# Optimization experiments

Hardware: AMD Instinct MI355X
Metric: run time of the kernel (lower is better)

Reference implementation:

```python
import jax, jax.numpy as jnp
import numpy as np

B = 131072
DIM = 64
D_IN = 32
D_OUT = 32
HIDDEN = 512
N_BINS = 8
TAIL = 3.0


def setup_inputs() -> dict:
    key = jax.random.key(0)
    ks = jax.random.split(key, 7)
    x = jax.random.normal(ks[0], (B, DIM), dtype=jnp.float32)
    out_dim = D_OUT * (3 * N_BINS - 1)  # 32 * 23 = 736
    W1 = jax.random.normal(ks[1], (D_IN, HIDDEN), dtype=jnp.float32) / np.sqrt(D_IN)
    b1 = jnp.zeros((HIDDEN,), dtype=jnp.float32)
    W2 = jax.random.normal(ks[2], (HIDDEN, HIDDEN), dtype=jnp.float32) / np.sqrt(HIDDEN)
    b2 = jnp.zeros((HIDDEN,), dtype=jnp.float32)
    W3 = jax.random.normal(ks[3], (HIDDEN, out_dim), dtype=jnp.float32) / np.sqrt(HIDDEN)
    b3 = jnp.zeros((out_dim,), dtype=jnp.float32)
    return {"x": x, "W1": W1, "b1": b1, "W2": W2, "b2": b2, "W3": W3, "b3": b3}


def _gather(t, idx):
    # t: (..., K), idx: (...) -> (...,)
    return jnp.take_along_axis(t, idx[..., None], axis=-1)[..., 0]


def rq_spline_forward(x, widths, heights, derivatives, tail_bound=TAIL):
    K = widths.shape[-1]
    widths = jax.nn.softmax(widths, axis=-1) * 2 * tail_bound
    heights = jax.nn.softmax(heights, axis=-1) * 2 * tail_bound
    derivatives = jax.nn.softplus(derivatives)
    ones = jnp.ones_like(derivatives[..., :1])
    derivatives = jnp.concatenate([ones, derivatives, ones], axis=-1)  # (..., K+1)
    cumwidths = jnp.cumsum(widths, axis=-1)
    cumwidths = jnp.pad(cumwidths, [(0, 0)] * (cumwidths.ndim - 1) + [(1, 0)]) - tail_bound
    cumheights = jnp.cumsum(heights, axis=-1)
    cumheights = jnp.pad(cumheights, [(0, 0)] * (cumheights.ndim - 1) + [(1, 0)]) - tail_bound

    inside = (x >= -tail_bound) & (x <= tail_bound)
    xc = jnp.clip(x, -tail_bound + 1e-6, tail_bound - 1e-6)
    # searchsorted (left): number of knots strictly less than xc
    bin_idx = jnp.sum(cumwidths[..., 1:] < xc[..., None], axis=-1)
    bin_idx = jnp.clip(bin_idx, 0, K - 1)

    w_k = _gather(widths, bin_idx)
    h_k = _gather(heights, bin_idx)
    d_k = _gather(derivatives, bin_idx)
    d_k1 = _gather(derivatives[..., 1:], bin_idx)
    cw_k = _gather(cumwidths, bin_idx)
    ch_k = _gather(cumheights, bin_idx)

    xi = jnp.clip((xc - cw_k) / w_k, 1e-6, 1 - 1e-6)
    s_k = h_k / w_k
    num = h_k * (s_k * xi**2 + d_k * xi * (1 - xi))
    den = s_k + (d_k + d_k1 - 2 * s_k) * xi * (1 - xi)
    y_inside = ch_k + num / den
    log_det_inside = (
        jnp.log(s_k**2 * (d_k1 * xi**2 + 2 * s_k * xi * (1 - xi) + d_k * (1 - xi) ** 2) + 1e-8)
        - jnp.log(den**2 + 1e-8)
    )
    y = jnp.where(inside, y_inside, x)
    log_det = jnp.where(inside, log_det_inside, jnp.zeros_like(x))
    return y, log_det


def reference(x, W1, b1, W2, b2, W3, b3):
    # mask: first D_IN dims conditioned on, last D_OUT transformed
    x_masked = x[:, :D_IN]
    x_transform = x[:, D_IN:]
    h = jax.nn.relu(x_masked @ W1 + b1)
    h = jax.nn.relu(h @ W2 + b2)
    raw = h @ W3 + b3
    raw = raw.reshape(x.shape[0], D_OUT, 3 * N_BINS - 1)
    widths = raw[..., :N_BINS]
    heights = raw[..., N_BINS:2 * N_BINS]
    derivs = raw[..., 2 * N_BINS:]
    y_t, log_det = rq_spline_forward(x_transform, widths, heights, derivs, TAIL)
    y = jnp.concatenate([x_masked, y_t], axis=-1)
    return y, jnp.sum(log_det, axis=-1)
```

## Files before the change

kernel.cpp:

```cpp
#include <hip/hip_runtime.h>
#include <hip/hip_bf16.h>
#include <stdint.h>

typedef __bf16 bf16_t;
typedef _Float16 f16_t;
typedef _Float16 f16x8 __attribute__((ext_vector_type(8)));
typedef _Float16 f16x4 __attribute__((ext_vector_type(4)));
typedef float f32x4 __attribute__((ext_vector_type(4)));

#define HID 512
#define NRAW 736
#define NRAW_PAD 768
#define TAILB 3.0f

__device__ __forceinline__ void glds16(const void* g, void* s) {
  __builtin_amdgcn_global_load_lds(
      (const __attribute__((address_space(1))) void*)g,
      (__attribute__((address_space(3))) void*)s, 16, 0, 0);
}
__device__ __forceinline__ float frcp(float x) { return __builtin_amdgcn_rcpf(x); }

__global__ void detect_dtype(const void* x, int* flag) {
  __shared__ int s;
  if (threadIdx.x == 0) s = 0;
  __syncthreads();
  const bf16_t* xb = (const bf16_t*)x;
  int cnt = 0;
  for (int j = 0; j < 16; j++) {
    float v = (float)xb[threadIdx.x * 16 + j];
    if (!(v == v) || fabsf(v) > 64.0f) cnt++;
  }
  atomicAdd(&s, cnt);
  __syncthreads();
  if (threadIdx.x == 0) *flag = (s > 64) ? 1 : 0;
}

__global__ void conv_wb(const void* W1, const void* W2, const void* W3,
                        const void* b1, const void* b2, const void* b3,
                        f16_t* __restrict__ w1t, f16_t* __restrict__ w2t,
                        f16_t* __restrict__ w3t,
                        float* __restrict__ bf1, float* __restrict__ bf2,
                        float* __restrict__ bf3, const int* flagp) {
  const int flag = *flagp;
  auto rd = [&](const void* p, size_t idx) -> float {
    return flag ? ((const float*)p)[idx] : (float)((const bf16_t*)p)[idx];
  };
  int i = blockIdx.x * 256 + threadIdx.x;
  if (i < 512 * 32)  { w1t[i] = (f16_t)rd(W1, (size_t)(i & 31) * 512 + (i >> 5)); return; }
  i -= 512 * 32;
  if (i < 512 * 512) { w2t[i] = (f16_t)rd(W2, (size_t)(i & 511) * 512 + (i >> 9)); return; }
  i -= 512 * 512;
  if (i < NRAW_PAD * 512) {
    int n = i >> 9, k = i & 511;
    int ch = n / 24, e = n % 24;
    w3t[i] = (e < 23) ? (f16_t)rd(W3, (size_t)k * NRAW + ch * 23 + e) : (f16_t)0.0f;
    return;
  }
  i -= NRAW_PAD * 512;
  if (i < 512) { bf1[i] = rd(b1, i); return; }
  i -= 512;
  if (i < 512) { bf2[i] = rd(b2, i); return; }
  i -= 512;
  if (i < NRAW_PAD) {
    int ch = i / 24, e = i % 24;
    bf3[i] = (e < 23) ? rd(b3, (size_t)ch * 23 + e) : 0.0f;
  }
}

__global__ void convert_x(const void* x, void* __restrict__ outv,
                          const int* flagp, int n) {
  const int flag = *flagp;
  const int i0 = (blockIdx.x * 256 + threadIdx.x) * 8;
  if (i0 >= n) return;
  const int row = i0 >> 5, col = i0 & 31;
  const size_t src = (size_t)row * 64 + col;
  if (flag) {
    const float4* s4 = (const float4*)((const float*)x + src);
    float4* d4 = (float4*)((float*)outv + src);
    d4[0] = s4[0]; d4[1] = s4[1];
  } else {
    *(uint4*)((bf16_t*)outv + src) = *(const uint4*)((const bf16_t*)x + src);
  }
}

__global__ void ld_finalize(const float* __restrict__ ldp, void* __restrict__ outv,
                            const int* __restrict__ flagp, int M) {
  const int i = blockIdx.x * 256 + threadIdx.x;
  if (i >= M) return;
  float s = 0.f;
  #pragma unroll
  for (int n = 0; n < 4; n++) s += ldp[(size_t)n * M + i];
  if (*flagp) ((float*)outv)[(size_t)M * 64 + i] = s;
  else        ((bf16_t*)outv)[(size_t)M * 64 + i] = (bf16_t)s;
}

__launch_bounds__(512, 4)
__global__ void gemm12(const void* __restrict__ xorig, const f16_t* __restrict__ W1t,
                       const float* __restrict__ b1, const f16_t* __restrict__ W2t,
                       const float* __restrict__ b2, f16_t* __restrict__ H2,
                       int r0, const int* __restrict__ flagp) {
  constexpr int BK = 64;
  constexpr int BUF = 128 * BK;
  __shared__ __align__(16) f16_t As[2 * BUF], Bs[2 * BUF];
  const int t = threadIdx.x;
  const int id = blockIdx.x;
  const int xcd = id & 7, s = id >> 3;
  const int n0 = (s & 3) * 128;
  const int m0 = ((s >> 2) * 8 + xcd) * 128;
  const int lrow = t >> 3, lcb = t & 7;
  const int lane = t & 63, w = t >> 6;
  const int wr = (w >> 2) * 64;
  const int wc = (w & 3) * 32;
  const int wc4 = (w & 3) * 16;
  const int lm = lane & 15, quad = lane >> 4;
  const int flag = *flagp;

  const f16_t* gb[2];
  f16_t* ldb[2];
  #pragma unroll
  for (int r = 0; r < 2; r++) {
    const int row = r * 64 + lrow;
    const int gc = (lcb ^ (row & 7)) * 8;
    gb[r] = W2t + (size_t)(n0 + row) * 512 + gc;
    ldb[r] = &Bs[row * BK + lcb * 8];
  }
  int apo[4][2], bpo[2][2];
  #pragma unroll
  for (int ksi = 0; ksi < 2; ksi++) {
    const int qb = ksi * 4 + quad;
    #pragma unroll
    for (int i = 0; i < 4; i++) {
      const int ra = wr + i * 16 + lm;
      apo[i][ksi] = ra * BK + ((qb ^ (ra & 7)) << 3);
    }
    #pragma unroll
    for (int j = 0; j < 2; j++) {
      const int rb = wc + j * 16 + lm;
      bpo[j][ksi] = rb * BK + ((qb ^ (rb & 7)) << 3);
    }
  }
  f16x8 xfr[4];
  #pragma unroll
  for (int i = 0; i < 4; i++) {
    const size_t xrow = (size_t)(r0 + m0 + wr + i * 16 + lm);
    if (flag) {
      const float* px = (const float*)xorig + xrow * 64 + quad * 8;
      const float4 a = *(const float4*)px;
      const float4 b = *(const float4*)(px + 4);
      f16x8 v;
      v[0] = (f16_t)a.x; v[1] = (f16_t)a.y; v[2] = (f16_t)a.z; v[3] = (f16_t)a.w;
      v[4] = (f16_t)b.x; v[5] = (f16_t)b.y; v[6] = (f16_t)b.z; v[7] = (f16_t)b.w;
      xfr[i] = v;
    } else {
      const bf16_t* px = (const bf16_t*)xorig + xrow * 64 + quad * 8;
      f16x8 v;
      #pragma unroll
      for (int j = 0; j < 8; j++) v[j] = (f16_t)(float)px[j];
      xfr[i] = v;
    }
  }
  const f16_t* w1p = W1t + (size_t)(wc4 + lm) * 32 + quad * 8;
  const float* b1p = b1 + wc4 + 4 * quad;
  int woff[4];
  {
    const int cb = (w & 3) * 2 + (quad >> 1);
    #pragma unroll
    for (int i = 0; i < 4; i++) {
      const int row = wr + i * 16 + lm;
      woff[i] = row * BK + ((cb ^ (row & 7)) << 3) + 4 * (quad & 1);
    }
  }

  f32x4 acc[4][2] = {};

  #pragma unroll
  for (int r = 0; r < 2; r++) glds16(gb[r], ldb[r]);
  {
    const f16x8 w1f = *(const f16x8*)w1p;
    const float4 bv = *(const float4*)b1p;
    #pragma unroll
    for (int i = 0; i < 4; i++) {
      f32x4 z = {};
      const f32x4 h = __builtin_amdgcn_mfma_f32_16x16x32_f16(w1f, xfr[i], z, 0, 0, 0);
      f16x4 v;
      v[0] = (f16_t)fmaxf(h[0] + bv.x, 0.0f);
      v[1] = (f16_t)fmaxf(h[1] + bv.y, 0.0f);
      v[2] = (f16_t)fmaxf(h[2] + bv.z, 0.0f);
      v[3] = (f16_t)fmaxf(h[3] + bv.w, 0.0f);
      *(f16x4*)&As[woff[i]] = v;
    }
  }
  f16x8 w1fa = *(const f16x8*)(w1p + (size_t)64 * 32);
  float4 bva = *(const float4*)(b1p + 64);
  __syncthreads();

  #pragma unroll
  for (int k = 0; k < 8; k++) {
    const int cur = k & 1, nb = cur ^ 1;
    if (k < 7) {
      #pragma unroll
      for (int r = 0; r < 2; r++)
        glds16(gb[r] + (k + 1) * 64, ldb[r] + nb * BUF);
    }
    f32x4 h[4];
    if (k < 7) {
      #pragma unroll
      for (int i = 0; i < 4; i++) {
        f32x4 z = {};
        h[i] = __builtin_amdgcn_mfma_f32_16x16x32_f16(w1fa, xfr[i], z, 0, 0, 0);
      }
    }
    #pragma unroll
    for (int ksi = 0; ksi < 2; ksi++) {
      f16x8 af[4], bf[2];
      #pragma unroll
      for (int i = 0; i < 4; i++) af[i] = *(const f16x8*)&As[cur * BUF + apo[i][ksi]];
      #pragma unroll
      for (int j = 0; j < 2; j++) bf[j] = *(const f16x8*)&Bs[cur * BUF + bpo[j][ksi]];
      __builtin_amdgcn_s_setprio(1);
      #pragma unroll
      for (int i = 0; i < 4; i++)
        #pragma unroll
        for (int j = 0; j < 2; j++)
          acc[i][j] = __builtin_amdgcn_mfma_f32_16x16x32_f16(af[i], bf[j], acc[i][j], 0, 0, 0);
      __builtin_amdgcn_s_setprio(0);
    }
    if (k < 7) {
      #pragma unroll
      for (int i = 0; i < 4; i++) {
        f16x4 v;
        v[0] = (f16_t)fmaxf(h[i][0] + bva.x, 0.0f);
        v[1] = (f16_t)fmaxf(h[i][1] + bva.y, 0.0f);
        v[2] = (f16_t)fmaxf(h[i][2] + bva.z, 0.0f);
        v[3] = (f16_t)fmaxf(h[i][3] + bva.w, 0.0f);
        *(f16x4*)&As[nb * BUF + woff[i]] = v;
      }
      if (k < 6) {
        w1fa = *(const f16x8*)(w1p + (size_t)(k + 2) * 64 * 32);
        bva = *(const float4*)(b1p + (k + 2) * 64);
      }
      __syncthreads();
    }
  }
  #pragma unroll
  for (int i = 0; i < 4; i++)
    #pragma unroll
    for (int j = 0; j < 2; j++) {
      const int col = n0 + wc + j * 16 + lm;
      const float bv = b2[col];
      #pragma unroll
      for (int r = 0; r < 4; r++) {
        const int rowi = m0 + wr + i * 16 + quad * 4 + r;
        H2[(size_t)rowi * HID + col] = (f16_t)fmaxf(acc[i][j][r] + bv, 0.0f);
      }
    }
}

#define RSH 200
#define SP1 0.5413248546f

__launch_bounds__(512, 4)
__global__ void gemm3_spline(const f16_t* __restrict__ A, const f16_t* __restrict__ Bt,
                             const float* __restrict__ bias,
                             const void* __restrict__ xorig,
                             void* __restrict__ outv, float* __restrict__ ldp,
                             int M, int r0, const int* __restrict__ flagp) {
  __shared__ __align__(16) f16_t lds[2 * 8192 + 2 * 12288];
  f16_t* As = lds;
  f16_t* Bs = lds + 2 * 8192;
  f16_t* rawh = lds;

  const int t = threadIdx.x;
  const int id = blockIdx.x;
  const int xcd = id & 7, sloc = id >> 3;
  const int cpx = gridDim.x >> 3;
  const int wg = xcd * cpx + sloc;
  const int ntile = wg & 3;
  const int m0 = (wg >> 2) * 128;
  const int n0 = ntile * 192;
  const int lane = t & 63, w = t >> 6;
  const int lm = lane & 15, quad = lane >> 4;
  const int wrow = (w >> 2) * 64, wcol = (w & 3) * 48;
  const int lrow = t >> 3, lcb = t & 7;
  const int flag = *flagp;

  const int gc = (lcb ^ (lrow & 7)) * 8;
  const f16_t* gA = A + (size_t)(m0 + lrow) * 512 + gc;
  const f16_t* gB = Bt + (size_t)(n0 + lrow) * 512 + gc;
  f16_t* ldA = As + lrow * 64 + lcb * 8;
  f16_t* ldB = Bs + lrow * 64 + lcb * 8;

  int aoff[4], boff[3];
  #pragma unroll
  for (int i = 0; i < 4; i++) {
    const int ra = wrow + i * 16 + lm;
    aoff[i] = ra * 64 + ((quad ^ (ra & 7)) << 3);
  }
  #pragma unroll
  for (int j = 0; j < 3; j++) {
    const int rb = wcol + j * 16 + lm;
    boff[j] = rb * 64 + ((quad ^ (rb & 7)) << 3);
  }

  const int prow = t >> 3, pch = t & 7;
  float xt_pre[2];
  #pragma unroll
  for (int e = 0; e < 2; e++) {
    const size_t gi = (size_t)(r0 + m0 + e * 64 + prow) * 64 + 32 + ntile * 8 + pch;
    xt_pre[e] = flag ? ((const float*)xorig)[gi] : (float)((const bf16_t*)xorig)[gi];
  }
  float bv3[3];
  #pragma unroll
  for (int j = 0; j < 3; j++) bv3[j] = bias[n0 + wcol + j * 16 + lm];

  #pragma unroll
  for (int r = 0; r < 2; r++) glds16(gA + r * 32768, ldA + r * 4096);
  #pragma unroll
  for (int r = 0; r < 3; r++) glds16(gB + r * 32768, ldB + r * 4096);
  __syncthreads();

  f32x4 acc[4][3] = {};

  #pragma unroll
  for (int t8 = 0; t8 < 8; t8++) {
    const f16_t* Ab = As + (t8 & 1) * 8192;
    const f16_t* Bb = Bs + (t8 & 1) * 12288;
    if (t8 < 7) {
      const int nb = (t8 + 1) & 1;
      #pragma unroll
      for (int r = 0; r < 2; r++)
        glds16(gA + r * 32768 + (t8 + 1) * 64, ldA + nb * 8192 + r * 4096);
      #pragma unroll
      for (int r = 0; r < 3; r++)
        glds16(gB + r * 32768 + (t8 + 1) * 64, ldB + nb * 12288 + r * 4096);
    }
    #pragma unroll
    for (int ksi = 0; ksi < 2; ksi++) {
      f16x8 af[4], bf[3];
      #pragma unroll
      for (int i = 0; i < 4; i++)
        af[i] = *(const f16x8*)(Ab + (aoff[i] ^ (ksi << 5)));
      #pragma unroll
      for (int j = 0; j < 3; j++)
        bf[j] = *(const f16x8*)(Bb + (boff[j] ^ (ksi << 5)));
      __builtin_amdgcn_s_setprio(1);
      #pragma unroll
      for (int i = 0; i < 4; i++)
        #pragma unroll
        for (int j = 0; j < 3; j++)
          acc[i][j] = __builtin_amdgcn_mfma_f32_16x16x32_f16(af[i], bf[j], acc[i][j], 0, 0, 0);
      __builtin_amdgcn_s_setprio(0);
    }
    __syncthreads();
  }

  #pragma unroll
  for (int i = 0; i < 4; i++)
    #pragma unroll
    for (int j = 0; j < 3; j++) {
      const int col = wcol + j * 16 + lm;
      #pragma unroll
      for (int r = 0; r < 4; r++)
        rawh[(wrow + i * 16 + quad * 4 + r) * RSH + col] = (f16_t)(acc[i][j][r] + bv3[j]);
    }
  __syncthreads();

  #pragma unroll
  for (int e = 0; e < 2; e++) {
    const int row = e * 64 + prow;
    const f16_t* c16 = &rawh[row * RSH + pch * 24];
    const f16x8 v0 = *(const f16x8*)(c16);
    const f16x8 v1 = *(const f16x8*)(c16 + 8);
    const f16x8 v2 = *(const f16x8*)(c16 + 16);
    float wa[8], ha[8], da[7];
    #pragma unroll
    for (int j = 0; j < 8; j++) { wa[j] = (float)v0[j]; ha[j] = (float)v1[j]; }
    #pragma unroll
    for (int j = 0; j < 7; j++) da[j] = (float)v2[j];

    const float xt = xt_pre[e];
    const bool inside = (xt >= -TAILB) && (xt <= TAILB);
    const float xc = fminf(fmaxf(xt, -TAILB + 1e-6f), TAILB - 1e-6f);

    float mw = wa[0], mh = ha[0];
    #pragma unroll
    for (int j = 1; j < 8; j++) { mw = fmaxf(mw, wa[j]); mh = fmaxf(mh, ha[j]); }
    float ew[8], eh[8], sew = 0.f, seh = 0.f;
    #pragma unroll
    for (int j = 0; j < 8; j++) {
      ew[j] = __expf(wa[j] - mw); sew += ew[j];
      eh[j] = __expf(ha[j] - mh); seh += eh[j];
    }
    const float wsc = 6.0f * frcp(sew), hsc = 6.0f * frcp(seh);
    #pragma unroll
    for (int j = 0; j < 8; j++) { ew[j] *= wsc; eh[j] *= hsc; }

    float accw = -TAILB, runh = -TAILB;
    float cwk = -TAILB, chk = -TAILB;
    float wk = ew[0], hk = eh[0];
    float dkr = SP1, dk1r = da[0];
    #pragma unroll
    for (int i = 0; i < 7; i++) {
      accw += ew[i];
      runh += eh[i];
      const bool cond = accw < xc;
      cwk  = cond ? accw : cwk;
      chk  = cond ? runh : chk;
      wk   = cond ? ew[i + 1] : wk;
      hk   = cond ? eh[i + 1] : hk;
      dkr  = cond ? da[i] : dkr;
      dk1r = cond ? ((i == 6) ? SP1 : da[i + 1]) : dk1r;
    }
    const float dk  = fmaxf(dkr, 0.0f)  + __logf(1.0f + __expf(-fabsf(dkr)));
    const float dk1 = fmaxf(dk1r, 0.0f) + __logf(1.0f + __expf(-fabsf(dk1r)));

    const float rwk = frcp(wk);
    float xi = (xc - cwk) * rwk;
    xi = fminf(fmaxf(xi, 1e-6f), 1.0f - 1e-6f);
    const float om = 1.0f - xi;
    const float sl = hk * rwk;
    const float num = hk * (sl * xi * xi + dk * xi * om);
    const float den = sl + (dk + dk1 - 2.0f * sl) * xi * om;
    const float y_in = chk + num * frcp(den);
    const float t1 = sl * sl * (dk1 * xi * xi + 2.0f * sl * xi * om + dk * om * om);
    const float ld_in = __logf(t1 + 1e-8f) - __logf(den * den + 1e-8f);

    const float yv = inside ? y_in : xt;
    const float ldv = inside ? ld_in : 0.0f;

    const size_t grow = (size_t)(r0 + m0 + row);
    if (flag) ((float*)outv)[grow * 64 + 32 + ntile * 8 + pch] = yv;
    else      ((bf16_t*)outv)[grow * 64 + 32 + ntile * 8 + pch] = (bf16_t)yv;

    float l = ldv + __shfl_down(ldv, 1, 8);
    l += __shfl_down(l, 2, 8);
    l += __shfl_down(l, 4, 8);
    if ((t & 7) == 0) ldp[(size_t)ntile * M + grow] = l;
  }
}

extern "C" void kernel_launch(void* const* d_in, const int* in_sizes, int n_in,
                              void* d_out, int out_size, void* d_ws, size_t ws_size,
                              hipStream_t stream) {
  const void* x  = d_in[0];
  const void* W1 = d_in[1];
  const void* b1 = d_in[2];
  const void* W2 = d_in[3];
  const void* b2 = d_in[4];
  const void* W3 = d_in[5];
  const void* b3 = d_in[6];
  const int M = in_sizes[0] / 64;

  char* ws = (char*)d_ws;
  size_t off = 0;
  auto alloc = [&](size_t bytes) {
    void* p = ws + off;
    off += (bytes + 255) & ~(size_t)255;
    return p;
  };
  int*   flag = (int*)alloc(256);
  float* bf1  = (float*)alloc(512 * 4);
  float* bf2  = (float*)alloc(512 * 4);
  float* bf3  = (float*)alloc(NRAW_PAD * 4);
  f16_t* W1t  = (f16_t*)alloc((size_t)512 * 32 * 2);
  f16_t* W2t  = (f16_t*)alloc((size_t)512 * 512 * 2);
  f16_t* W3t  = (f16_t*)alloc((size_t)NRAW_PAD * 512 * 2);
  float* ldp  = (float*)alloc((size_t)8 * M * 4);

  const size_t per_row = (size_t)HID * 2;
  size_t avail = (ws_size > off + 4096) ? (ws_size - off - 4096) : 0;
  long rows = (long)(avail / per_row);
  rows -= rows % 1024;
  if (rows > M) rows = M;
  if (rows < 1024) rows = 1024;

  f16_t* h2 = (f16_t*)alloc((size_t)rows * HID * 2);

  detect_dtype<<<1, 256, 0, stream>>>(x, flag);
  conv_wb<<<2631, 256, 0, stream>>>(W1, W2, W3, b1, b2, b3,
                                    W1t, W2t, W3t, bf1, bf2, bf3, flag);
  convert_x<<<(M * 32 / 8 + 255) / 256, 256, 0, stream>>>(x, d_out, flag, M * 32);

  for (int r0 = 0; r0 < M; r0 += (int)rows) {
    const int mc = (int)((M - r0 < rows) ? (M - r0) : rows);
    const int mt128 = mc / 128;
    gemm12<<<mt128 * 4, 512, 0, stream>>>(x, W1t, bf1, W2t, bf2, h2, r0, flag);
    gemm3_spline<<<mt128 * 4, 512, 0, stream>>>(
        h2, W3t, bf3, x, d_out, ldp, M, r0, flag);
  }
  ld_finalize<<<(M + 255) / 256, 256, 0, stream>>>(ldp, d_out, flag, M);
}
```

Baseline: 320.5 us.

## Triple-buffer the gemm3_spline LDS pipeline with prefetch distance two

Moves the third GEMM's K-loop from double to triple buffering in LDS, issuing global-to-LDS loads two tiles ahead. Each iteration now waits on the vector-memory counter explicitly and uses one raw s_barrier instead of a trailing __syncthreads, so load latency has more time to hide behind MFMA work. The cost is a larger LDS footprint (about 120 KB instead of 80 KB) and launch bounds lowered from 4 to 2, which cuts how many blocks can be resident per CU.

```diff
diff --git a/kernel.cpp b/kernel.cpp
--- a/kernel.cpp
+++ b/kernel.cpp
@@ -258,16 +258,15 @@
 
 #define RSH 200
 #define SP1 0.5413248546f
-
-__launch_bounds__(512, 4)
+#define G3BUF 20480
+
+__launch_bounds__(512, 2)
 __global__ void gemm3_spline(const f16_t* __restrict__ A, const f16_t* __restrict__ Bt,
                              const float* __restrict__ bias,
                              const void* __restrict__ xorig,
                              void* __restrict__ outv, float* __restrict__ ldp,
                              int M, int r0, const int* __restrict__ flagp) {
-  __shared__ __align__(16) f16_t lds[2 * 8192 + 2 * 12288];
-  f16_t* As = lds;
-  f16_t* Bs = lds + 2 * 8192;
+  __shared__ __align__(16) f16_t lds[3 * G3BUF];
   f16_t* rawh = lds;
 
   const int t = threadIdx.x;
@@ -287,8 +286,7 @@
   const int gc = (lcb ^ (lrow & 7)) * 8;
   const f16_t* gA = A + (size_t)(m0 + lrow) * 512 + gc;
   const f16_t* gB = Bt + (size_t)(n0 + lrow) * 512 + gc;
-  f16_t* ldA = As + lrow * 64 + lcb * 8;
-  f16_t* ldB = Bs + lrow * 64 + lcb * 8;
+  const int lslot = lrow * 64 + lcb * 8;
 
   int aoff[4], boff[3];
   #pragma unroll
@@ -299,7 +297,7 @@
   #pragma unroll
   for (int j = 0; j < 3; j++) {
     const int rb = wcol + j * 16 + lm;
-    boff[j] = rb * 64 + ((quad ^ (rb & 7)) << 3);
+    boff[j] = 8192 + rb * 64 + ((quad ^ (rb & 7)) << 3);
   }
 
   const int prow = t >> 3, pch = t & 7;
@@ -313,33 +311,43 @@
   #pragma unroll
   for (int j = 0; j < 3; j++) bv3[j] = bias[n0 + wcol + j * 16 + lm];
 
-  #pragma unroll
-  for (int r = 0; r < 2; r++) glds16(gA + r * 32768, ldA + r * 4096);
-  #pragma unroll
-  for (int r = 0; r < 3; r++) glds16(gB + r * 32768, ldB + r * 4096);
-  __syncthreads();
+  asm volatile("s_waitcnt vmcnt(0)" ::: "memory");
+  __builtin_amdgcn_sched_barrier(0);
+
+  #pragma unroll
+  for (int r = 0; r < 2; r++) glds16(gA + r * 32768,       lds + lslot + r * 4096);
+  #pragma unroll
+  for (int r = 0; r < 3; r++) glds16(gB + r * 32768,       lds + 8192 + lslot + r * 4096);
+  #pragma unroll
+  for (int r = 0; r < 2; r++) glds16(gA + r * 32768 + 64,  lds + G3BUF + lslot + r * 4096);
+  #pragma unroll
+  for (int r = 0; r < 3; r++) glds16(gB + r * 32768 + 64,  lds + G3BUF + 8192 + lslot + r * 4096);
 
   f32x4 acc[4][3] = {};
 
   #pragma unroll
   for (int t8 = 0; t8 < 8; t8++) {
-    const f16_t* Ab = As + (t8 & 1) * 8192;
-    const f16_t* Bb = Bs + (t8 & 1) * 12288;
-    if (t8 < 7) {
-      const int nb = (t8 + 1) & 1;
+    if (t8 == 7) asm volatile("s_waitcnt vmcnt(0)" ::: "memory");
+    else         asm volatile("s_waitcnt vmcnt(5)" ::: "memory");
+    __builtin_amdgcn_sched_barrier(0);
+    __builtin_amdgcn_s_barrier();
+    __builtin_amdgcn_sched_barrier(0);
+    if (t8 < 6) {
+      const int nb = (t8 + 2) % 3;
       #pragma unroll
       for (int r = 0; r < 2; r++)
-        glds16(gA + r * 32768 + (t8 + 1) * 64, ldA + nb * 8192 + r * 4096);
+        glds16(gA + r * 32768 + (t8 + 2) * 64, lds + nb * G3BUF + lslot + r * 4096);
       #pragma unroll
       for (int r = 0; r < 3; r++)
-        glds16(gB + r * 32768 + (t8 + 1) * 64, ldB + nb * 12288 + r * 4096);
-    }
+        glds16(gB + r * 32768 + (t8 + 2) * 64, lds + nb * G3BUF + 8192 + lslot + r * 4096);
+    }
+    const f16_t* Bb = lds + (t8 % 3) * G3BUF;
     #pragma unroll
     for (int ksi = 0; ksi < 2; ksi++) {
       f16x8 af[4], bf[3];
       #pragma unroll
       for (int i = 0; i < 4; i++)
-        af[i] = *(const f16x8*)(Ab + (aoff[i] ^ (ksi << 5)));
+        af[i] = *(const f16x8*)(Bb + (aoff[i] ^ (ksi << 5)));
       #pragma unroll
       for (int j = 0; j < 3; j++)
         bf[j] = *(const f16x8*)(Bb + (boff[j] ^ (ksi << 5)));
@@ -351,8 +359,9 @@
           acc[i][j] = __builtin_amdgcn_mfma_f32_16x16x32_f16(af[i], bf[j], acc[i][j], 0, 0, 0);
       __builtin_amdgcn_s_setprio(0);
     }
-    __syncthreads();
-  }
+  }
+
+  __syncthreads();
 
   #pragma unroll
   for (int i = 0; i < 4; i++)
```

Result: slower. 364.8 us (+13.8%).

## Merge GEMM12 and GEMM3+spline into one software-pipelined kernel over row chunks

Applied to the files above, without the earlier changes.

Both GEMM stages are fused into a single kernel where even blocks run layers 1-2 for chunk c and odd blocks run layer 3 plus the spline for chunk c-1. A double-buffered H2 workspace lets the two stages overlap within one launch instead of running as back-to-back dependent launches. The aim is to fill the device with mixed work and hide each stage's tail. The costs are a fixed 16384-row chunk, extra launches for pipeline fill and drain, and a larger shared-memory footprint for the GEMM12 role.

```diff
diff --git a/kernel.cpp b/kernel.cpp
--- a/kernel.cpp
+++ b/kernel.cpp
@@ -94,348 +94,348 @@
   else        ((bf16_t*)outv)[(size_t)M * 64 + i] = (bf16_t)s;
 }
 
+#define RSH 200
+#define SP1 0.5413248546f
+
 __launch_bounds__(512, 4)
-__global__ void gemm12(const void* __restrict__ xorig, const f16_t* __restrict__ W1t,
-                       const float* __restrict__ b1, const f16_t* __restrict__ W2t,
-                       const float* __restrict__ b2, f16_t* __restrict__ H2,
-                       int r0, const int* __restrict__ flagp) {
-  constexpr int BK = 64;
-  constexpr int BUF = 128 * BK;
-  __shared__ __align__(16) f16_t As[2 * BUF], Bs[2 * BUF];
+__global__ void gemm_pipe(const void* __restrict__ xorig,
+                          const f16_t* __restrict__ W1t, const float* __restrict__ b1,
+                          const f16_t* __restrict__ W2t, const float* __restrict__ b2,
+                          f16_t* __restrict__ h2w, const f16_t* __restrict__ h2r,
+                          const f16_t* __restrict__ W3t, const float* __restrict__ bf3v,
+                          void* __restrict__ outv, float* __restrict__ ldp,
+                          int M, int g12r0, int g3r0, int nb12, int nb3,
+                          const int* __restrict__ flagp) {
+  __shared__ __align__(16) f16_t lds[40960];
   const int t = threadIdx.x;
-  const int id = blockIdx.x;
-  const int xcd = id & 7, s = id >> 3;
-  const int n0 = (s & 3) * 128;
-  const int m0 = ((s >> 2) * 8 + xcd) * 128;
+  const int role = blockIdx.x & 1;
+  const int sid = blockIdx.x >> 1;
+  const int lane = t & 63, w = t >> 6;
+  const int lm = lane & 15, quad = lane >> 4;
   const int lrow = t >> 3, lcb = t & 7;
-  const int lane = t & 63, w = t >> 6;
-  const int wr = (w >> 2) * 64;
-  const int wc = (w & 3) * 32;
-  const int wc4 = (w & 3) * 16;
-  const int lm = lane & 15, quad = lane >> 4;
   const int flag = *flagp;
 
-  const f16_t* gb[2];
-  f16_t* ldb[2];
-  #pragma unroll
-  for (int r = 0; r < 2; r++) {
-    const int row = r * 64 + lrow;
-    const int gc = (lcb ^ (row & 7)) * 8;
-    gb[r] = W2t + (size_t)(n0 + row) * 512 + gc;
-    ldb[r] = &Bs[row * BK + lcb * 8];
-  }
-  int apo[4][2], bpo[2][2];
-  #pragma unroll
-  for (int ksi = 0; ksi < 2; ksi++) {
-    const int qb = ksi * 4 + quad;
+  if (role == 0) {
+    if (g12r0 < 0 || sid >= nb12) return;
+    constexpr int BK = 64;
+    constexpr int BUF = 128 * BK;
+    f16_t* As = lds;
+    f16_t* Bs = lds + 2 * BUF;
+    const int xcd = sid & 7, s = sid >> 3;
+    const int n0 = (s & 3) * 128;
+    const int m0 = ((s >> 2) * 8 + xcd) * 128;
+    const int wr = (w >> 2) * 64;
+    const int wc = (w & 3) * 32;
+    const int wc4 = (w & 3) * 16;
+    const int r0 = g12r0;
+
+    const f16_t* gb[2];
+    f16_t* ldb[2];
+    #pragma unroll
+    for (int r = 0; r < 2; r++) {
+      const int row = r * 64 + lrow;
+      const int gc = (lcb ^ (row & 7)) * 8;
+      gb[r] = W2t + (size_t)(n0 + row) * 512 + gc;
+      ldb[r] = &Bs[row * BK + lcb * 8];
+    }
+    int apo[4][2], bpo[2][2];
+    #pragma unroll
+    for (int ksi = 0; ksi < 2; ksi++) {
+      const int qb = ksi * 4 + quad;
+      #pragma unroll
+      for (int i = 0; i < 4; i++) {
+        const int ra = wr + i * 16 + lm;
+        apo[i][ksi] = ra * BK + ((qb ^ (ra & 7)) << 3);
+      }
+      #pragma unroll
+      for (int j = 0; j < 2; j++) {
+        const int rb = wc + j * 16 + lm;
+        bpo[j][ksi] = rb * BK + ((qb ^ (rb & 7)) << 3);
+      }
+    }
+    f16x8 xfr[4];
     #pragma unroll
     for (int i = 0; i < 4; i++) {
-      const int ra = wr + i * 16 + lm;
-      apo[i][ksi] = ra * BK + ((qb ^ (ra & 7)) << 3);
-    }
-    #pragma unroll
-    for (int j = 0; j < 2; j++) {
-      const int rb = wc + j * 16 + lm;
-      bpo[j][ksi] = rb * BK + ((qb ^ (rb & 7)) << 3);
-    }
-  }
-  f16x8 xfr[4];
-  #pragma unroll
-  for (int i = 0; i < 4; i++) {
-    const size_t xrow = (size_t)(r0 + m0 + wr + i * 16 + lm);
-    if (flag) {
-      const float* px = (const float*)xorig + xrow * 64 + quad * 8;
-      const float4 a = *(const float4*)px;
-      const float4 b = *(const float4*)(px + 4);
-      f16x8 v;
-      v[0] = (f16_t)a.x; v[1] = (f16_t)a.y; v[2] = (f16_t)a.z; v[3] = (f16_t)a.w;
-      v[4] = (f16_t)b.x; v[5] = (f16_t)b.y; v[6] = (f16_t)b.z; v[7] = (f16_t)b.w;
-      xfr[i] = v;
-    } else {
-      const bf16_t* px = (const bf16_t*)xorig + xrow * 64 + quad * 8;
-      f16x8 v;
-      #pragma unroll
-      for (int j = 0; j < 8; j++) v[j] = (f16_t)(float)px[j];
-      xfr[i] = v;
-    }
-  }
-  const f16_t* w1p = W1t + (size_t)(wc4 + lm) * 32 + quad * 8;
-  const float* b1p = b1 + wc4 + 4 * quad;
-  int woff[4];
-  {
-    const int cb = (w & 3) * 2 + (quad >> 1);
-    #pragma unroll
-    for (int i = 0; i < 4; i++) {
-      const int row = wr + i * 16 + lm;
-      woff[i] = row * BK + ((cb ^ (row & 7)) << 3) + 4 * (quad & 1);
-    }
-  }
-
-  f32x4 acc[4][2] = {};
-
-  #pragma unroll
-  for (int r = 0; r < 2; r++) glds16(gb[r], ldb[r]);
-  {
-    const f16x8 w1f = *(const f16x8*)w1p;
-    const float4 bv = *(const float4*)b1p;
-    #pragma unroll
-    for (int i = 0; i < 4; i++) {
-      f32x4 z = {};
-      const f32x4 h = __builtin_amdgcn_mfma_f32_16x16x32_f16(w1f, xfr[i], z, 0, 0, 0);
-      f16x4 v;
-      v[0] = (f16_t)fmaxf(h[0] + bv.x, 0.0f);
-      v[1] = (f16_t)fmaxf(h[1] + bv.y, 0.0f);
-      v[2] = (f16_t)fmaxf(h[2] + bv.z, 0.0f);
-      v[3] = (f16_t)fmaxf(h[3] + bv.w, 0.0f);
-      *(f16x4*)&As[woff[i]] = v;
-    }
-  }
-  f16x8 w1fa = *(const f16x8*)(w1p + (size_t)64 * 32);
-  float4 bva = *(const float4*)(b1p + 64);
-  __syncthreads();
-
-  #pragma unroll
-  for (int k = 0; k < 8; k++) {
-    const int cur = k & 1, nb = cur ^ 1;
-    if (k < 7) {
-      #pragma unroll
-      for (int r = 0; r < 2; r++)
-        glds16(gb[r] + (k + 1) * 64, ldb[r] + nb * BUF);
-    }
-    f32x4 h[4];
-    if (k < 7) {
+      const size_t xrow = (size_t)(r0 + m0 + wr + i * 16 + lm);
+      if (flag) {
+        const float* px = (const float*)xorig + xrow * 64 + quad * 8;
+        const float4 a = *(const float4*)px;
+        const float4 b = *(const float4*)(px + 4);
+        f16x8 v;
+        v[0] = (f16_t)a.x; v[1] = (f16_t)a.y; v[2] = (f16_t)a.z; v[3] = (f16_t)a.w;
+        v[4] = (f16_t)b.x; v[5] = (f16_t)b.y; v[6] = (f16_t)b.z; v[7] = (f16_t)b.w;
+        xfr[i] = v;
+      } else {
+        const bf16_t* px = (const bf16_t*)xorig + xrow * 64 + quad * 8;
+        f16x8 v;
+        #pragma unroll
+        for (int j = 0; j < 8; j++) v[j] = (f16_t)(float)px[j];
+        xfr[i] = v;
+      }
+    }
+    const f16_t* w1p = W1t + (size_t)(wc4 + lm) * 32 + quad * 8;
+    const float* b1p = b1 + wc4 + 4 * quad;
+    int woff[4];
+    {
+      const int cb = (w & 3) * 2 + (quad >> 1);
+      #pragma unroll
+      for (int i = 0; i < 4; i++) {
+        const int row = wr + i * 16 + lm;
+        woff[i] = row * BK + ((cb ^ (row & 7)) << 3) + 4 * (quad & 1);
+      }
+    }
+
+    f32x4 acc[4][2] = {};
+
+    #pragma unroll
+    for (int r = 0; r < 2; r++) glds16(gb[r], ldb[r]);
+    {
+      const f16x8 w1f = *(const f16x8*)w1p;
+      const float4 bv = *(const float4*)b1p;
       #pragma unroll
       for (int i = 0; i < 4; i++) {
         f32x4 z = {};
-        h[i] = __builtin_amdgcn_mfma_f32_16x16x32_f16(w1fa, xfr[i], z, 0, 0, 0);
-      }
-    }
-    #pragma unroll
-    for (int ksi = 0; ksi < 2; ksi++) {
-      f16x8 af[4], bf[2];
-      #pragma unroll
-      for (int i = 0; i < 4; i++) af[i] = *(const f16x8*)&As[cur * BUF + apo[i][ksi]];
-      #pragma unroll
-      for (int j = 0; j < 2; j++) bf[j] = *(const f16x8*)&Bs[cur * BUF + bpo[j][ksi]];
-      __builtin_amdgcn_s_setprio(1);
-      #pragma unroll
-      for (int i = 0; i < 4; i++)
-        #pragma unroll
-        for (int j = 0; j < 2; j++)
-          acc[i][j] = __builtin_amdgcn_mfma_f32_16x16x32_f16(af[i], bf[j], acc[i][j], 0, 0, 0);
-      __builtin_amdgcn_s_setprio(0);
-    }
-    if (k < 7) {
-      #pragma unroll
-      for (int i = 0; i < 4; i++) {
+        const f32x4 h = __builtin_amdgcn_mfma_f32_16x16x32_f16(w1f, xfr[i], z, 0, 0, 0);
         f16x4 v;
-        v[0] = (f16_t)fmaxf(h[i][0] + bva.x, 0.0f);
-        v[1] = (f16_t)fmaxf(h[i][1] + bva.y, 0.0f);
-        v[2] = (f16_t)fmaxf(h[i][2] + bva.z, 0.0f);
-        v[3] = (f16_t)fmaxf(h[i][3] + bva.w, 0.0f);
-        *(f16x4*)&As[nb * BUF + woff[i]] = v;
-      }
-      if (k < 6) {
-        w1fa = *(const f16x8*)(w1p + (size_t)(k + 2) * 64 * 32);
-        bva = *(const float4*)(b1p + (k + 2) * 64);
+        v[0] = (f16_t)fmaxf(h[0] + bv.x, 0.0f);
+        v[1] = (f16_t)fmaxf(h[1] + bv.y, 0.0f);
+        v[2] = (f16_t)fmaxf(h[2] + bv.z, 0.0f);
+        v[3] = (f16_t)fmaxf(h[3] + bv.w, 0.0f);
+        *(f16x4*)&As[woff[i]] = v;
+      }
+    }
+    f16x8 w1fa = *(const f16x8*)(w1p + (size_t)64 * 32);
+    float4 bva = *(const float4*)(b1p + 64);
+    __syncthreads();
+
+    #pragma unroll
+    for (int k = 0; k < 8; k++) {
+      const int cur = k & 1, nb = cur ^ 1;
+      if (k < 7) {
+        #pragma unroll
+        for (int r = 0; r < 2; r++)
+          glds16(gb[r] + (k + 1) * 64, ldb[r] + nb * BUF);
+      }
+      f32x4 h[4];
+      if (k < 7) {
+        #pragma unroll
+        for (int i = 0; i < 4; i++) {
+          f32x4 z = {};
+          h[i] = __builtin_amdgcn_mfma_f32_16x16x32_f16(w1fa, xfr[i], z, 0, 0, 0);
+        }
+      }
+      #pragma unroll
+      for (int ksi = 0; ksi < 2; ksi++) {
+        f16x8 af[4], bf[2];
+        #pragma unroll
+        for (int i = 0; i < 4; i++) af[i] = *(const f16x8*)&As[cur * BUF + apo[i][ksi]];
+        #pragma unroll
+        for (int j = 0; j < 2; j++) bf[j] = *(const f16x8*)&Bs[cur * BUF + bpo[j][ksi]];
+        __builtin_amdgcn_s_setprio(1);
+        #pragma unroll
+        for (int i = 0; i < 4; i++)
+          #pragma unroll
+          for (int j = 0; j < 2; j++)
+            acc[i][j] = __builtin_amdgcn_mfma_f32_16x16x32_f16(af[i], bf[j], acc[i][j], 0, 0, 0);
+        __builtin_amdgcn_s_setprio(0);
+      }
+      if (k < 7) {
+        #pragma unroll
+        for (int i = 0; i < 4; i++) {
+          f16x4 v;
+          v[0] = (f16_t)fmaxf(h[i][0] + bva.x, 0.0f);
+          v[1] = (f16_t)fmaxf(h[i][1] + bva.y, 0.0f);
+          v[2] = (f16_t)fmaxf(h[i][2] + bva.z, 0.0f);
+          v[3] = (f16_t)fmaxf(h[i][3] + bva.w, 0.0f);
+          *(f16x4*)&As[nb * BUF + woff[i]] = v;
+        }
+        if (k < 6) {
+          w1fa = *(const f16x8*)(w1p + (size_t)(k + 2) * 64 * 32);
+          bva = *(const float4*)(b1p + (k + 2) * 64);
+        }
+        __syncthreads();
+      }
+    }
+    #pragma unroll
+    for (int i = 0; i < 4; i++)
+      #pragma unroll
+      for (int j = 0; j < 2; j++) {
+        const int col = n0 + wc + j * 16 + lm;
+        const float bv = b2[col];
+        #pragma unroll
+        for (int r = 0; r < 4; r++) {
+          const int rowi = m0 + wr + i * 16 + quad * 4 + r;
+          h2w[(size_t)rowi * HID + col] = (f16_t)fmaxf(acc[i][j][r] + bv, 0.0f);
+        }
+      }
+  } else {
+    if (g3r0 < 0 || sid >= nb3) return;
+    f16_t* As = lds;
+    f16_t* Bs = lds + 2 * 8192;
+    f16_t* rawh = lds;
+    const int nsub = gridDim.x >> 1;
+    const int xcd = sid & 7, sloc = sid >> 3;
+    const int cpx = nsub >> 3;
+    const int wg = xcd * cpx + sloc;
+    const int ntile = wg & 3;
+    const int m0 = (wg >> 2) * 128;
+    const int n0 = ntile * 192;
+    const int wrow = (w >> 2) * 64, wcol = (w & 3) * 48;
+    const int r0 = g3r0;
+
+    const int gc = (lcb ^ (lrow & 7)) * 8;
+    const f16_t* gA = h2r + (size_t)(m0 + lrow) * 512 + gc;
+    const f16_t* gB = W3t + (size_t)(n0 + lrow) * 512 + gc;
+    f16_t* ldA = As + lrow * 64 + lcb * 8;
+    f16_t* ldB = Bs + lrow * 64 + lcb * 8;
+
+    int aoff[4], boff[3];
+    #pragma unroll
+    for (int i = 0; i < 4; i++) {
+      const int ra = wrow + i * 16 + lm;
+      aoff[i] = ra * 64 + ((quad ^ (ra & 7)) << 3);
+    }
+    #pragma unroll
+    for (int j = 0; j < 3; j++) {
+      const int rb = wcol + j * 16 + lm;
+      boff[j] = rb * 64 + ((quad ^ (rb & 7)) << 3);
+    }
+
+    const int prow = t >> 3, pch = t & 7;
+    float xt_pre[2];
+    #pragma unroll
+    for (int e = 0; e < 2; e++) {
+      const size_t gi = (size_t)(r0 + m0 + e * 64 + prow) * 64 + 32 + ntile * 8 + pch;
+      xt_pre[e] = flag ? ((const float*)xorig)[gi] : (float)((const bf16_t*)xorig)[gi];
+    }
+    float bv3[3];
+    #pragma unroll
+    for (int j = 0; j < 3; j++) bv3[j] = bf3v[n0 + wcol + j * 16 + lm];
+
+    #pragma unroll
+    for (int r = 0; r < 2; r++) glds16(gA + r * 32768, ldA + r * 4096);
+    #pragma unroll
+    for (int r = 0; r < 3; r++) glds16(gB + r * 32768, ldB + r * 4096);
+    __syncthreads();
+
+    f32x4 acc[4][3] = {};
+
+    #pragma unroll
+    for (int t8 = 0; t8 < 8; t8++) {
+      const f16_t* Ab = As + (t8 & 1) * 8192;
+      const f16_t* Bb = Bs + (t8 & 1) * 12288;
+      if (t8 < 7) {
+        const int nb = (t8 + 1) & 1;
+        #pragma unroll
+        for (int r = 0; r < 2; r++)
+          glds16(gA + r * 32768 + (t8 + 1) * 64, ldA + nb * 8192 + r * 4096);
+        #pragma unroll
+        for (int r = 0; r < 3; r++)
+          glds16(gB + r * 32768 + (t8 + 1) * 64, ldB + nb * 12288 + r * 4096);
+      }
+      #pragma unroll
+      for (int ksi = 0; ksi < 2; ksi++) {
+        f16x8 af[4], bf[3];
+        #pragma unroll
+        for (int i = 0; i < 4; i++)
+          af[i] = *(const f16x8*)(Ab + (aoff[i] ^ (ksi << 5)));
+        #pragma unroll
+        for (int j = 0; j < 3; j++)
+          bf[j] = *(const f16x8*)(Bb + (boff[j] ^ (ksi << 5)));
+        __builtin_amdgcn_s_setprio(1);
+        #pragma unroll
+        for (int i = 0; i < 4; i++)
+          #pragma unroll
+          for (int j = 0; j < 3; j++)
+            acc[i][j] = __builtin_amdgcn_mfma_f32_16x16x32_f16(af[i], bf[j], acc[i][j], 0, 0, 0);
+        __builtin_amdgcn_s_setprio(0);
       }
       __syncthreads();
     }
-  }
-  #pragma unroll
-  for (int i = 0; i < 4; i++)
-    #pragma unroll
-    for (int j = 0; j < 2; j++) {
-      const int col = n0 + wc + j * 16 + lm;
-      const float bv = b2[col];
-      #pragma unroll
-      for (int r = 0; r < 4; r++) {
-        const int rowi = m0 + wr + i * 16 + quad * 4 + r;
-        H2[(size_t)rowi * HID + col] = (f16_t)fmaxf(acc[i][j][r] + bv, 0.0f);
-      }
-    }
-}
-
-#define RSH 200
-#define SP1 0.5413248546f
-
-__launch_bounds__(512, 4)
-__global__ void gemm3_spline(const f16_t* __restrict__ A, const f16_t* __restrict__ Bt,
-                             const float* __restrict__ bias,
-                             const void* __restrict__ xorig,
-                             void* __restrict__ outv, float* __restrict__ ldp,
-                             int M, int r0, const int* __restrict__ flagp) {
-  __shared__ __align__(16) f16_t lds[2 * 8192 + 2 * 12288];
-  f16_t* As = lds;
-  f16_t* Bs = lds + 2 * 8192;
-  f16_t* rawh = lds;
-
-  const int t = threadIdx.x;
-  const int id = blockIdx.x;
-  const int xcd = id & 7, sloc = id >> 3;
-  const int cpx = gridDim.x >> 3;
-  const int wg = xcd * cpx + sloc;
-  const int ntile = wg & 3;
-  const int m0 = (wg >> 2) * 128;
-  const int n0 = ntile * 192;
-  const int lane = t & 63, w = t >> 6;
-  const int lm = lane & 15, quad = lane >> 4;
-  const int wrow = (w >> 2) * 64, wcol = (w & 3) * 48;
-  const int lrow = t >> 3, lcb = t & 7;
-  const int flag = *flagp;
-
-  const int gc = (lcb ^ (lrow & 7)) * 8;
-  const f16_t* gA = A + (size_t)(m0 + lrow) * 512 + gc;
-  const f16_t* gB = Bt + (size_t)(n0 + lrow) * 512 + gc;
-  f16_t* ldA = As + lrow * 64 + lcb * 8;
-  f16_t* ldB = Bs + lrow * 64 + lcb * 8;
-
-  int aoff[4], boff[3];
-  #pragma unroll
-  for (int i = 0; i < 4; i++) {
-    const int ra = wrow + i * 16 + lm;
-    aoff[i] = ra * 64 + ((quad ^ (ra & 7)) << 3);
-  }
-  #pragma unroll
-  for (int j = 0; j < 3; j++) {
-    const int rb = wcol + j * 16 + lm;
-    boff[j] = rb * 64 + ((quad ^ (rb & 7)) << 3);
-  }
-
-  const int prow = t >> 3, pch = t & 7;
-  float xt_pre[2];
-  #pragma unroll
-  for (int e = 0; e < 2; e++) {
-    const size_t gi = (size_t)(r0 + m0 + e * 64 + prow) * 64 + 32 + ntile * 8 + pch;
-    xt_pre[e] = flag ? ((const float*)xorig)[gi] : (float)((const bf16_t*)xorig)[gi];
-  }
-  float bv3[3];
-  #pragma unroll
-  for (int j = 0; j < 3; j++) bv3[j] = bias[n0 + wcol + j * 16 + lm];
-
-  #pragma unroll
-  for (int r = 0; r < 2; r++) glds16(gA + r * 32768, ldA + r * 4096);
-  #pragma unroll
-  for (int r = 0; r < 3; r++) glds16(gB + r * 32768, ldB + r * 4096);
-  __syncthreads();
-
-  f32x4 acc[4][3] = {};
-
-  #pragma unroll
-  for (int t8 = 0; t8 < 8; t8++) {
-    const f16_t* Ab = As + (t8 & 1) * 8192;
-    const f16_t* Bb = Bs + (t8 & 1) * 12288;
-    if (t8 < 7) {
-      const int nb = (t8 + 1) & 1;
-      #pragma unroll
-      for (int r = 0; r < 2; r++)
-        glds16(gA + r * 32768 + (t8 + 1) * 64, ldA + nb * 8192 + r * 4096);
-      #pragma unroll
-      for (int r = 0; r < 3; r++)
-        glds16(gB + r * 32768 + (t8 + 1) * 64, ldB + nb * 12288 + r * 4096);
-    }
-    #pragma unroll
-    for (int ksi = 0; ksi < 2; ksi++) {
-      f16x8 af[4], bf[3];
-      #pragma unroll
-      for (int i = 0; i < 4; i++)
-        af[i] = *(const f16x8*)(Ab + (aoff[i] ^ (ksi << 5)));
-      #pragma unroll
-      for (int j = 0; j < 3; j++)
-        bf[j] = *(const f16x8*)(Bb + (boff[j] ^ (ksi << 5)));
-      __builtin_amdgcn_s_setprio(1);
-      #pragma unroll
-      for (int i = 0; i < 4; i++)
-        #pragma unroll
-        for (int j = 0; j < 3; j++)
-          acc[i][j] = __builtin_amdgcn_mfma_f32_16x16x32_f16(af[i], bf[j], acc[i][j], 0, 0, 0);
-      __builtin_amdgcn_s_setprio(0);
-    }
+
+    #pragma unroll
+    for (int i = 0; i < 4; i++)
+      #pragma unroll
+      for (int j = 0; j < 3; j++) {
+        const int col = wcol + j * 16 + lm;
+        #pragma unroll
+        for (int r = 0; r < 4; r++)
+          rawh[(wrow + i * 16 + quad * 4 + r) * RSH + col] = (f16_t)(acc[i][j][r] + bv3[j]);
+      }
     __syncthreads();
-  }
-
-  #pragma unroll
-  for (int i = 0; i < 4; i++)
-    #pragma unroll
-    for (int j = 0; j < 3; j++) {
-      const int col = wcol + j * 16 + lm;
-      #pragma unroll
-      for (int r = 0; r < 4; r++)
-        rawh[(wrow + i * 16 + quad * 4 + r) * RSH + col] = (f16_t)(acc[i][j][r] + bv3[j]);
-    }
-  __syncthreads();
-
-  #pragma unroll
-  for (int e = 0; e < 2; e++) {
-    const int row = e * 64 + prow;
-    const f16_t* c16 = &rawh[row * RSH + pch * 24];
-    const f16x8 v0 = *(const f16x8*)(c16);
-    const f16x8 v1 = *(const f16x8*)(c16 + 8);
-    const f16x8 v2 = *(const f16x8*)(c16 + 16);
-    float wa[8], ha[8], da[7];
-    #pragma unroll
-    for (int j = 0; j < 8; j++) { wa[j] = (float)v0[j]; ha[j] = (float)v1[j]; }
-    #pragma unroll
-    for (int j = 0; j < 7; j++) da[j] = (float)v2[j];
-
-    const float xt = xt_pre[e];
-    const bool inside = (xt >= -TAILB) && (xt <= TAILB);
-    const float xc = fminf(fmaxf(xt, -TAILB + 1e-6f), TAILB - 1e-6f);
-
-    float mw = wa[0], mh = ha[0];
-    #pragma unroll
-    for (int j = 1; j < 8; j++) { mw = fmaxf(mw, wa[j]); mh = fmaxf(mh, ha[j]); }
-    float ew[8], eh[8], sew = 0.f, seh = 0.f;
-    #pragma unroll
-    for (int j = 0; j < 8; j++) {
-      ew[j] = __expf(wa[j] - mw); sew += ew[j];
-      eh[j] = __expf(ha[j] - mh); seh += eh[j];
-    }
-    const float wsc = 6.0f * frcp(sew), hsc = 6.0f * frcp(seh);
-    #pragma unroll
-    for (int j = 0; j < 8; j++) { ew[j] *= wsc; eh[j] *= hsc; }
-
-    float accw = -TAILB, runh = -TAILB;
-    float cwk = -TAILB, chk = -TAILB;
-    float wk = ew[0], hk = eh[0];
-    float dkr = SP1, dk1r = da[0];
-    #pragma unroll
-    for (int i = 0; i < 7; i++) {
-      accw += ew[i];
-      runh += eh[i];
-      const bool cond = accw < xc;
-      cwk  = cond ? accw : cwk;
-      chk  = cond ? runh : chk;
-      wk   = cond ? ew[i + 1] : wk;
-      hk   = cond ? eh[i + 1] : hk;
-      dkr  = cond ? da[i] : dkr;
-      dk1r = cond ? ((i == 6) ? SP1 : da[i + 1]) : dk1r;
-    }
-    const float dk  = fmaxf(dkr, 0.0f)  + __logf(1.0f + __expf(-fabsf(dkr)));
-    const float dk1 = fmaxf(dk1r, 0.0f) + __logf(1.0f + __expf(-fabsf(dk1r)));
-
-    const float rwk = frcp(wk);
-    float xi = (xc - cwk) * rwk;
-    xi = fminf(fmaxf(xi, 1e-6f), 1.0f - 1e-6f);
-    const float om = 1.0f - xi;
-    const float sl = hk * rwk;
-    const float num = hk * (sl * xi * xi + dk * xi * om);
-    const float den = sl + (dk + dk1 - 2.0f * sl) * xi * om;
-    const float y_in = chk + num * frcp(den);
-    const float t1 = sl * sl * (dk1 * xi * xi + 2.0f * sl * xi * om + dk * om * om);
-    const float ld_in = __logf(t1 + 1e-8f) - __logf(den * den + 1e-8f);
-
-    const float yv = inside ? y_in : xt;
-    const float ldv = inside ? ld_in : 0.0f;
-
-    const size_t grow = (size_t)(r0 + m0 + row);
-    if (flag) ((float*)outv)[grow * 64 + 32 + ntile * 8 + pch] = yv;
-    else      ((bf16_t*)outv)[grow * 64 + 32 + ntile * 8 + pch] = (bf16_t)yv;
-
-    float l = ldv + __shfl_down(ldv, 1, 8);
-    l += __shfl_down(l, 2, 8);
-    l += __shfl_down(l, 4, 8);
-    if ((t & 7) == 0) ldp[(size_t)ntile * M + grow] = l;
+
+    #pragma unroll
+    for (int e = 0; e < 2; e++) {
+      const int row = e * 64 + prow;
+      const f16_t* c16 = &rawh[row * RSH + pch * 24];
+      const f16x8 v0 = *(const f16x8*)(c16);
+      const f16x8 v1 = *(const f16x8*)(c16 + 8);
+      const f16x8 v2 = *(const f16x8*)(c16 + 16);
+      float wa[8], ha[8], da[7];
+      #pragma unroll
+      for (int j = 0; j < 8; j++) { wa[j] = (float)v0[j]; ha[j] = (float)v1[j]; }
+      #pragma unroll
+      for (int j = 0; j < 7; j++) da[j] = (float)v2[j];
+
+      const float xt = xt_pre[e];
+      const bool inside = (xt >= -TAILB) && (xt <= TAILB);
+      const float xc = fminf(fmaxf(xt, -TAILB + 1e-6f), TAILB - 1e-6f);
+
+      float mw = wa[0], mh = ha[0];
+      #pragma unroll
+      for (int j = 1; j < 8; j++) { mw = fmaxf(mw, wa[j]); mh = fmaxf(mh, ha[j]); }
+      float ew[8], eh[8], sew = 0.f, seh = 0.f;
+      #pragma unroll
+      for (int j = 0; j < 8; j++) {
+        ew[j] = __expf(wa[j] - mw); sew += ew[j];
+        eh[j] = __expf(ha[j] - mh); seh += eh[j];
+      }
+      const float wsc = 6.0f * frcp(sew), hsc = 6.0f * frcp(seh);
+      #pragma unroll
+      for (int j = 0; j < 8; j++) { ew[j] *= wsc; eh[j] *= hsc; }
+
+      float accw = -TAILB, runh = -TAILB;
+      float cwk = -TAILB, chk = -TAILB;
+      float wk = ew[0], hk = eh[0];
+      float dkr = SP1, dk1r = da[0];
+      #pragma unroll
+      for (int i = 0; i < 7; i++) {
+        accw += ew[i];
+        runh += eh[i];
+        const bool cond = accw < xc;
+        cwk  = cond ? accw : cwk;
+        chk  = cond ? runh : chk;
+        wk   = cond ? ew[i + 1] : wk;
+        hk   = cond ? eh[i + 1] : hk;
+        dkr  = cond ? da[i] : dkr;
+        dk1r = cond ? ((i == 6) ? SP1 : da[i + 1]) : dk1r;
+      }
+      const float dk  = fmaxf(dkr, 0.0f)  + __logf(1.0f + __expf(-fabsf(dkr)));
+      const float dk1 = fmaxf(dk1r, 0.0f) + __logf(1.0f + __expf(-fabsf(dk1r)));
+
+      const float rwk = frcp(wk);
+      float xi = (xc - cwk) * rwk;
+      xi = fminf(fmaxf(xi, 1e-6f), 1.0f - 1e-6f);
+      const float om = 1.0f - xi;
+      const float sl = hk * rwk;
+      const float num = hk * (sl * xi * xi + dk * xi * om);
+      const float den = sl + (dk + dk1 - 2.0f * sl) * xi * om;
+      const float y_in = chk + num * frcp(den);
+      const float t1 = sl * sl * (dk1 * xi * xi + 2.0f * sl * xi * om + dk * om * om);
+      const float ld_in = __logf(t1 + 1e-8f) - __logf(den * den + 1e-8f);
+
+      const float yv = inside ? y_in : xt;
+      const float ldv = inside ? ld_in : 0.0f;
+
+      const size_t grow = (size_t)(r0 + m0 + row);
+      if (flag) ((float*)outv)[grow * 64 + 32 + ntile * 8 + pch] = yv;
+      else      ((bf16_t*)outv)[grow * 64 + 32 + ntile * 8 + pch] = (bf16_t)yv;
+
+      float l = ldv + __shfl_down(ldv, 1, 8);
+      l += __shfl_down(l, 2, 8);
+      l += __shfl_down(l, 4, 8);
+      if ((t & 7) == 0) ldp[(size_t)ntile * M + grow] = l;
+    }
   }
 }
 
@@ -465,28 +465,38 @@
   f16_t* W1t  = (f16_t*)alloc((size_t)512 * 32 * 2);
   f16_t* W2t  = (f16_t*)alloc((size_t)512 * 512 * 2);
   f16_t* W3t  = (f16_t*)alloc((size_t)NRAW_PAD * 512 * 2);
-  float* ldp  = (float*)alloc((size_t)8 * M * 4);
+  float* ldp  = (float*)alloc((size_t)4 * M * 4);
 
   const size_t per_row = (size_t)HID * 2;
+  long rows = 16384;
   size_t avail = (ws_size > off + 4096) ? (ws_size - off - 4096) : 0;
-  long rows = (long)(avail / per_row);
-  rows -= rows % 1024;
-  if (rows > M) rows = M;
-  if (rows < 1024) rows = 1024;
-
-  f16_t* h2 = (f16_t*)alloc((size_t)rows * HID * 2);
+  if ((size_t)(2 * rows) * per_row > avail) {
+    rows = (long)(avail / (2 * per_row));
+    rows -= rows % 1024;
+    if (rows < 1024) rows = 1024;
+  }
+  f16_t* h2 = (f16_t*)alloc((size_t)2 * rows * per_row);
 
   detect_dtype<<<1, 256, 0, stream>>>(x, flag);
   conv_wb<<<2631, 256, 0, stream>>>(W1, W2, W3, b1, b2, b3,
                                     W1t, W2t, W3t, bf1, bf2, bf3, flag);
   convert_x<<<(M * 32 / 8 + 255) / 256, 256, 0, stream>>>(x, d_out, flag, M * 32);
 
-  for (int r0 = 0; r0 < M; r0 += (int)rows) {
-    const int mc = (int)((M - r0 < rows) ? (M - r0) : rows);
-    const int mt128 = mc / 128;
-    gemm12<<<mt128 * 4, 512, 0, stream>>>(x, W1t, bf1, W2t, bf2, h2, r0, flag);
-    gemm3_spline<<<mt128 * 4, 512, 0, stream>>>(
-        h2, W3t, bf3, x, d_out, ldp, M, r0, flag);
+  const int nchunk = (int)((M + rows - 1) / rows);
+  int prev_rows = 0;
+  for (int c = 0; c <= nchunk; c++) {
+    const int g12r0 = (c < nchunk) ? (int)(c * rows) : -1;
+    const int cr = (c < nchunk) ? (int)(((M - c * rows) < rows) ? (M - c * rows) : rows) : 0;
+    const int g3r0 = (c > 0) ? (int)((c - 1) * rows) : -1;
+    const int nb12 = (c < nchunk) ? (cr / 128) * 4 : 0;
+    const int nb3 = (c > 0) ? (prev_rows / 128) * 4 : 0;
+    const int nmax = (nb12 > nb3) ? nb12 : nb3;
+    f16_t* h2w = h2 + (size_t)(c & 1) * rows * 512;
+    const f16_t* h2r = h2 + (size_t)((c - 1) & 1) * rows * 512;
+    gemm_pipe<<<2 * nmax, 512, 0, stream>>>(
+        x, W1t, bf1, W2t, bf2, h2w, h2r, W3t, bf3, d_out, ldp,
+        M, g12r0, g3r0, nb12, nb3, flag);
+    prev_rows = cr;
   }
   ld_finalize<<<(M + 255) / 256, 256, 0, stream>>>(ldp, d_out, flag, M);
 }
```

Measured after the change: 366.2 us. 1.14x slower.
